# Optimization experiments

Hardware: AMD Instinct MI355X
Metric: run time of the kernel (lower is better)

The kernel has to match this reference:

```python
import jax, jax.numpy as jnp
import numpy as np

B, S, H = 32, 2048, 1024


def setup_inputs() -> dict:
    key = jax.random.key(0)
    k1, k2, k3, k4, k5 = jax.random.split(key, 5)
    # scale linear weights like torch default init (~U(-1/sqrt(fan_in),..)); normal*small is fine for a numeric baseline
    return {
        "hidden": jax.random.normal(k1, (B, H), dtype=jnp.float32),
        "encoder_outputs": jax.random.normal(k2, (B, S, H), dtype=jnp.float32),
        "attn_w": jax.random.normal(k3, (H, 2 * H), dtype=jnp.float32) * (1.0 / np.sqrt(2 * H)),
        "attn_b": jax.random.normal(k4, (H,), dtype=jnp.float32) * (1.0 / np.sqrt(2 * H)),
        "v_w": jax.random.normal(k5, (1, H), dtype=jnp.float32) * (1.0 / np.sqrt(H)),
    }


def reference(hidden, encoder_outputs, attn_w, attn_b, v_w):
    # hidden: [B,H]; encoder_outputs: [B,S,H]
    # torch: cat((hidden repeated over S, enc), dim=2) @ attn_w.T + attn_b
    # Split attn_w columns: first H cols act on hidden, last H cols on enc.
    # Avoids materializing the repeated/concatenated [B,S,2H] tensor.
    Hdim = hidden.shape[-1]
    Wh = attn_w[:, :Hdim]   # [H, H] applied to hidden
    We = attn_w[:, Hdim:]   # [H, H] applied to encoder outputs
    # [B,1,H] + [B,S,H] + [H] -> tanh -> [B,S,H]
    e = jnp.tanh((hidden @ Wh.T)[:, None, :] + jnp.einsum('bsh,kh->bsk', encoder_outputs, We) + attn_b)
    scores = jnp.einsum('bsh,h->bs', e, v_w[0])          # [B,S], v has no bias
    attn_weights = jax.nn.softmax(scores, axis=1)        # softmax over source positions (dim=1)
    context = jnp.einsum('bs,bsh->bh', attn_weights, encoder_outputs)  # [B,H]
    output = jnp.concatenate([context, hidden], axis=1)  # [B,2H]
    return output, attn_weights[..., None]               # match torch shapes: [B,2H], [B,S,1]
```

## Files before the change

### kernel.cpp

```cpp
#include <hip/hip_runtime.h>
#include <stdint.h>

#define BATCH 32
#define SEQ   2048
#define HDIM  1024

typedef short short8 __attribute__((ext_vector_type(8)));
typedef float f32x4 __attribute__((ext_vector_type(4)));

__device__ __forceinline__ unsigned short f2b(float f) {
    unsigned u = __float_as_uint(f);
    u += 0x7FFFu + ((u >> 16) & 1u);
    return (unsigned short)(u >> 16);
}
__device__ __forceinline__ unsigned pk_bf16(float a, float b) {
    return __builtin_amdgcn_perm(__float_as_uint(b), __float_as_uint(a), 0x07060302u);
}
__device__ __forceinline__ float fast_tanh(float x) {
    float ex = __expf(2.0f * x);
    return 1.0f - 2.0f / (ex + 1.0f);
}
__device__ __forceinline__ void gl2lds16(const unsigned short* g, unsigned short* l) {
    __builtin_amdgcn_global_load_lds(
        (const __attribute__((address_space(1))) unsigned int*)g,
        (__attribute__((address_space(3))) unsigned int*)l, 16, 0, 0);
}

__global__ __launch_bounds__(256) void prep_kernel(
    const float* __restrict__ hidden, const float* __restrict__ attn_w,
    const float* __restrict__ attn_b, unsigned short* __restrict__ we_bf,
    float* __restrict__ qb, float* __restrict__ scores) {
    int k = blockIdx.x;
    int tid = threadIdx.x;

    if (tid < 64) scores[(size_t)k * 64 + tid] = 0.0f;

    {
        const float4* src = (const float4*)(attn_w + (size_t)k * 2048 + 1024);
        float4 v = src[tid];
        ushort4 o;
        o.x = f2b(v.x); o.y = f2b(v.y); o.z = f2b(v.z); o.w = f2b(v.w);
        ((ushort4*)(we_bf + (size_t)k * HDIM))[tid] = o;
    }

    float part[BATCH];
#pragma unroll
    for (int b = 0; b < BATCH; ++b) part[b] = 0.0f;
    const float* wrow = attn_w + (size_t)k * 2048;
    for (int h = tid; h < HDIM; h += 256) {
        float w = wrow[h];
#pragma unroll
        for (int b = 0; b < BATCH; ++b) part[b] += w * hidden[b * HDIM + h];
    }
    __shared__ float red[4][BATCH];
    int lane = tid & 63, wv = tid >> 6;
#pragma unroll
    for (int b = 0; b < BATCH; ++b) {
        float v = part[b];
        v += __shfl_xor(v, 1);  v += __shfl_xor(v, 2);  v += __shfl_xor(v, 4);
        v += __shfl_xor(v, 8);  v += __shfl_xor(v, 16); v += __shfl_xor(v, 32);
        if (lane == 0) red[wv][b] = v;
    }
    __syncthreads();
    if (tid < BATCH) {
        float v = red[0][tid] + red[1][tid] + red[2][tid] + red[3][tid] + attn_b[k];
        qb[(size_t)tid * HDIM + k] = v;
    }
}

__global__ __launch_bounds__(256) void convert_kernel(
    const float* __restrict__ enc, unsigned short* __restrict__ enc_bf) {
    int id = blockIdx.x;
    int m = id >> 2, g = id & 3;
    int tid = threadIdx.x;
    int r = tid >> 1, h = tid & 1;
    const float* src = enc + ((size_t)m * 128 + r) * HDIM;
    int r7 = r & 7;
#pragma unroll
    for (int k4 = 0; k4 < 4; ++k4) {
        int kt = g * 4 + k4;
        unsigned short* img =
            enc_bf + ((size_t)m * 16 + kt) * 8192 + r * 64 + h * 32;
#pragma unroll
        for (int p = 0; p < 4; ++p) {
            int c = (4 * h + p) ^ r7;
            const float4* s = (const float4*)(src + kt * 64 + c * 8);
            float4 x = s[0], y = s[1];
            uint4 o;
            o.x = pk_bf16(x.x, x.y); o.y = pk_bf16(x.z, x.w);
            o.z = pk_bf16(y.x, y.y); o.w = pk_bf16(y.z, y.w);
            *(uint4*)(img + p * 8) = o;
        }
    }
}

__global__ __launch_bounds__(256, 3) void score_gemm_kernel(
    const unsigned short* __restrict__ enc_bf,
    const unsigned short* __restrict__ we_bf,
    const float* __restrict__ qb, const float* __restrict__ v_w,
    float* __restrict__ scores) {
    __shared__ __align__(16) unsigned short As[8192];
    __shared__ __align__(16) unsigned short Bs[8192];

    int tid  = threadIdx.x;
    int lane = tid & 63, w = tid >> 6;
    int wm = w & 1, wn = w >> 1;
    int i15 = lane & 15, q = lane >> 4;

    int raw   = blockIdx.x;
    int i     = raw >> 3;
    int ntile = i & 7;
    int mtile = (raw & 7) * 64 + (i >> 3);
    int n0 = ntile * 128;
    long gm0 = (long)mtile * 128;
    int b = mtile >> 4;

    int brow_in = lane >> 3;
    int bchunk  = (lane & 7) ^ ((lane >> 3) & 7);
    const unsigned short* Bg =
        we_bf + (size_t)(n0 + w * 32 + brow_in) * HDIM + bchunk * 8;
    unsigned short* Bd = Bs + (w * 32) * 64 + lane * 8;

    const unsigned short* Atile = enc_bf + (size_t)mtile * 16 * 8192;
    int aoff = w * 2048 + lane * 8;

    f32x4 acc[4][4];
#pragma unroll
    for (int mt = 0; mt < 4; ++mt)
#pragma unroll
        for (int nt = 0; nt < 4; ++nt) acc[mt][nt] = (f32x4)0.0f;

    int arow0 = wm * 64 + i15;
    int brow0 = wn * 64 + i15;

#define STAGE(KT) do {                                                        \
        const unsigned short* bsrc = Bg + (size_t)(KT) * 64;                  \
        gl2lds16(bsrc,                     Bd);                               \
        gl2lds16(bsrc + (size_t)8  * HDIM, Bd + 512);                         \
        gl2lds16(bsrc + (size_t)16 * HDIM, Bd + 1024);                        \
        gl2lds16(bsrc + (size_t)24 * HDIM, Bd + 1536);                        \
        const unsigned short* asrc = Atile + (size_t)(KT) * 8192 + aoff;      \
        unsigned short* adst = As + aoff;                                     \
        gl2lds16(asrc,        adst);                                          \
        gl2lds16(asrc + 512,  adst + 512);                                    \
        gl2lds16(asrc + 1024, adst + 1024);                                   \
        gl2lds16(asrc + 1536, adst + 1536);                                   \
    } while (0)

    STAGE(0);
    __syncthreads();

    for (int kt = 0; kt < 16; ++kt) {
#pragma unroll
        for (int kk = 0; kk < 2; ++kk) {
            int xr = ((kk * 4 + q) ^ (i15 & 7)) * 8;
            short8 af[4], bf[4];
#pragma unroll
            for (int mt = 0; mt < 4; ++mt)
                af[mt] = *(const short8*)(As + (arow0 + mt * 16) * 64 + xr);
#pragma unroll
            for (int nt = 0; nt < 4; ++nt)
                bf[nt] = *(const short8*)(Bs + (brow0 + nt * 16) * 64 + xr);
#pragma unroll
            for (int mt = 0; mt < 4; ++mt)
#pragma unroll
                for (int nt = 0; nt < 4; ++nt)
                    acc[mt][nt] = __builtin_amdgcn_mfma_f32_16x16x32_bf16(
                        af[mt], bf[nt], acc[mt][nt], 0, 0, 0);
        }
        if (kt < 15) {
            __syncthreads();
            STAGE(kt + 1);
            __syncthreads();
        }
    }
#undef STAGE

    float sc[4][4];
#pragma unroll
    for (int mt = 0; mt < 4; ++mt)
#pragma unroll
        for (int r = 0; r < 4; ++r) sc[mt][r] = 0.0f;

#pragma unroll
    for (int nt = 0; nt < 4; ++nt) {
        int n = n0 + wn * 64 + nt * 16 + i15;
        float qv = qb[(size_t)b * HDIM + n];
        float vv = v_w[n];
#pragma unroll
        for (int mt = 0; mt < 4; ++mt)
#pragma unroll
            for (int r = 0; r < 4; ++r)
                sc[mt][r] += vv * fast_tanh(acc[mt][nt][r] + qv);
    }
#pragma unroll
    for (int mt = 0; mt < 4; ++mt)
#pragma unroll
        for (int r = 0; r < 4; ++r) {
            float v = sc[mt][r];
            v += __shfl_xor(v, 1); v += __shfl_xor(v, 2);
            v += __shfl_xor(v, 4); v += __shfl_xor(v, 8);
            if (i15 == 0)
                atomicAdd(&scores[gm0 + wm * 64 + mt * 16 + q * 4 + r], v);
        }
}

__global__ __launch_bounds__(256) void softmax_kernel(
    const float* __restrict__ scores, const float* __restrict__ hidden,
    float* out) {
    int b = blockIdx.x, tid = threadIdx.x;
    const float* srow = scores + (size_t)b * SEQ;
    __shared__ float redm[4];
    __shared__ float reds[4];
    int lane = tid & 63, wv = tid >> 6;

    float loc[8];
    float m = -1e30f;
#pragma unroll
    for (int i = 0; i < 8; ++i) {
        loc[i] = srow[tid + i * 256];
        m = fmaxf(m, loc[i]);
    }
#pragma unroll
    for (int d = 1; d < 64; d <<= 1) m = fmaxf(m, __shfl_xor(m, d));
    if (lane == 0) redm[wv] = m;
    __syncthreads();
    m = fmaxf(fmaxf(redm[0], redm[1]), fmaxf(redm[2], redm[3]));

    float sum = 0.0f;
#pragma unroll
    for (int i = 0; i < 8; ++i) {
        float e = __expf(loc[i] - m);
        loc[i] = e;
        sum += e;
    }
#pragma unroll
    for (int d = 1; d < 64; d <<= 1) sum += __shfl_xor(sum, d);
    if (lane == 0) reds[wv] = sum;
    __syncthreads();
    sum = reds[0] + reds[1] + reds[2] + reds[3];
    float inv = 1.0f / sum;

#pragma unroll
    for (int i = 0; i < 8; ++i)
        out[BATCH * SEQ + (size_t)b * SEQ + tid + i * 256] = loc[i] * inv;

    for (int i = tid; i < HDIM; i += 256) {
        out[(size_t)b * 2048 + i] = 0.0f;
        out[(size_t)b * 2048 + 1024 + i] = hidden[(size_t)b * HDIM + i];
    }
}

__global__ __launch_bounds__(256) void context_kernel(
    const float* __restrict__ enc, const float* __restrict__ weights_src,
    float* out) {
    int id = blockIdx.x;
    int scid = id & 15, b = id >> 4;
    int tid = threadIdx.x;
    __shared__ float wl[128];
    if (tid < 128)
        wl[tid] = weights_src[BATCH * SEQ + (size_t)b * SEQ + scid * 128 + tid];
    __syncthreads();
    const float* ebase = enc + ((size_t)(b * SEQ + scid * 128)) * HDIM + tid * 4;
    float a0 = 0.f, a1 = 0.f, a2 = 0.f, a3 = 0.f;
    float b0 = 0.f, b1 = 0.f, b2 = 0.f, b3 = 0.f;
#pragma unroll 4
    for (int s = 0; s < 64; ++s) {
        float4 e0 = *(const float4*)(ebase + (size_t)s * HDIM);
        float4 e1 = *(const float4*)(ebase + (size_t)(s + 64) * HDIM);
        float w0 = wl[s], w1 = wl[s + 64];
        a0 += w0 * e0.x; a1 += w0 * e0.y; a2 += w0 * e0.z; a3 += w0 * e0.w;
        b0 += w1 * e1.x; b1 += w1 * e1.y; b2 += w1 * e1.z; b3 += w1 * e1.w;
    }
    float* o = out + (size_t)b * 2048 + tid * 4;
    atomicAdd(o + 0, a0 + b0); atomicAdd(o + 1, a1 + b1);
    atomicAdd(o + 2, a2 + b2); atomicAdd(o + 3, a3 + b3);
}

extern "C" void kernel_launch(void* const* d_in, const int* in_sizes, int n_in,
                              void* d_out, int out_size, void* d_ws, size_t ws_size,
                              hipStream_t stream) {
    const float* hidden = (const float*)d_in[0];
    const float* enc    = (const float*)d_in[1];
    const float* attn_w = (const float*)d_in[2];
    const float* attn_b = (const float*)d_in[3];
    const float* v_w    = (const float*)d_in[4];
    float* out = (float*)d_out;

    char* ws = (char*)d_ws;
    unsigned short* enc_bf = (unsigned short*)ws;
    unsigned short* we_bf  = (unsigned short*)(ws + (size_t)134217728);
    float* qb     = (float*)(ws + (size_t)134217728 + 2097152);
    float* scores = (float*)(ws + (size_t)134217728 + 2097152 + 131072);

    prep_kernel<<<1024, 256, 0, stream>>>(hidden, attn_w, attn_b, we_bf, qb, scores);
    convert_kernel<<<2048, 256, 0, stream>>>(enc, enc_bf);
    score_gemm_kernel<<<4096, 256, 0, stream>>>(enc_bf, we_bf, qb, v_w, scores);
    softmax_kernel<<<32, 256, 0, stream>>>(scores, hidden, out);
    context_kernel<<<512, 256, 0, stream>>>(enc, out, out);
}
```

Baseline: 649.6 us.

## Merge prep and convert kernels, move softmax normalization into context kernel

Fuses the bf16 conversion of encoder outputs and the weight/query prep into one launch so the two independent workloads share a grid. The softmax kernel now only computes per-row max and inverse sum, and the context kernel recomputes the normalized weights and writes them out, dropping a full-row write and read. The GEMM launch bound goes from 3 to 5 blocks per CU, which may force register spilling.

```diff
diff --git a/kernel.cpp b/kernel.cpp
--- a/kernel.cpp
+++ b/kernel.cpp
@@ -26,13 +26,40 @@
         (__attribute__((address_space(3))) unsigned int*)l, 16, 0, 0);
 }
 
-__global__ __launch_bounds__(256) void prep_kernel(
+__global__ __launch_bounds__(256) void prep_convert_kernel(
     const float* __restrict__ hidden, const float* __restrict__ attn_w,
-    const float* __restrict__ attn_b, unsigned short* __restrict__ we_bf,
+    const float* __restrict__ attn_b, const float* __restrict__ enc,
+    unsigned short* __restrict__ we_bf, unsigned short* __restrict__ enc_bf,
     float* __restrict__ qb, float* __restrict__ scores) {
-    int k = blockIdx.x;
+    int bid = blockIdx.x;
     int tid = threadIdx.x;
-
+    __shared__ float red[4][BATCH];
+
+    if (bid < 2048) {
+        int m = bid >> 2, g = bid & 3;
+        int r = tid >> 1, h = tid & 1;
+        const float* src = enc + ((size_t)m * 128 + r) * HDIM;
+        int r7 = r & 7;
+#pragma unroll
+        for (int k4 = 0; k4 < 4; ++k4) {
+            int kt = g * 4 + k4;
+            unsigned short* img =
+                enc_bf + ((size_t)m * 16 + kt) * 8192 + r * 64 + h * 32;
+#pragma unroll
+            for (int p = 0; p < 4; ++p) {
+                int c = (4 * h + p) ^ r7;
+                const float4* s = (const float4*)(src + kt * 64 + c * 8);
+                float4 x = s[0], y = s[1];
+                uint4 o;
+                o.x = pk_bf16(x.x, x.y); o.y = pk_bf16(x.z, x.w);
+                o.z = pk_bf16(y.x, y.y); o.w = pk_bf16(y.z, y.w);
+                *(uint4*)(img + p * 8) = o;
+            }
+        }
+        return;
+    }
+
+    int k = bid - 2048;
     if (tid < 64) scores[(size_t)k * 64 + tid] = 0.0f;
 
     {
@@ -52,7 +79,6 @@
 #pragma unroll
         for (int b = 0; b < BATCH; ++b) part[b] += w * hidden[b * HDIM + h];
     }
-    __shared__ float red[4][BATCH];
     int lane = tid & 63, wv = tid >> 6;
 #pragma unroll
     for (int b = 0; b < BATCH; ++b) {
@@ -68,33 +94,7 @@
     }
 }
 
-__global__ __launch_bounds__(256) void convert_kernel(
-    const float* __restrict__ enc, unsigned short* __restrict__ enc_bf) {
-    int id = blockIdx.x;
-    int m = id >> 2, g = id & 3;
-    int tid = threadIdx.x;
-    int r = tid >> 1, h = tid & 1;
-    const float* src = enc + ((size_t)m * 128 + r) * HDIM;
-    int r7 = r & 7;
-#pragma unroll
-    for (int k4 = 0; k4 < 4; ++k4) {
-        int kt = g * 4 + k4;
-        unsigned short* img =
-            enc_bf + ((size_t)m * 16 + kt) * 8192 + r * 64 + h * 32;
-#pragma unroll
-        for (int p = 0; p < 4; ++p) {
-            int c = (4 * h + p) ^ r7;
-            const float4* s = (const float4*)(src + kt * 64 + c * 8);
-            float4 x = s[0], y = s[1];
-            uint4 o;
-            o.x = pk_bf16(x.x, x.y); o.y = pk_bf16(x.z, x.w);
-            o.z = pk_bf16(y.x, y.y); o.w = pk_bf16(y.z, y.w);
-            *(uint4*)(img + p * 8) = o;
-        }
-    }
-}
-
-__global__ __launch_bounds__(256, 3) void score_gemm_kernel(
+__global__ __launch_bounds__(256, 5) void score_gemm_kernel(
     const unsigned short* __restrict__ enc_bf,
     const unsigned short* __restrict__ we_bf,
     const float* __restrict__ qb, const float* __restrict__ v_w,
@@ -205,9 +205,9 @@
         }
 }
 
-__global__ __launch_bounds__(256) void softmax_kernel(
+__global__ __launch_bounds__(256) void softmax_stats_kernel(
     const float* __restrict__ scores, const float* __restrict__ hidden,
-    float* out) {
+    float* __restrict__ stats, float* out) {
     int b = blockIdx.x, tid = threadIdx.x;
     const float* srow = scores + (size_t)b * SEQ;
     __shared__ float redm[4];
@@ -229,21 +229,16 @@
 
     float sum = 0.0f;
 #pragma unroll
-    for (int i = 0; i < 8; ++i) {
-        float e = __expf(loc[i] - m);
-        loc[i] = e;
-        sum += e;
-    }
+    for (int i = 0; i < 8; ++i) sum += __expf(loc[i] - m);
 #pragma unroll
     for (int d = 1; d < 64; d <<= 1) sum += __shfl_xor(sum, d);
     if (lane == 0) reds[wv] = sum;
     __syncthreads();
-    sum = reds[0] + reds[1] + reds[2] + reds[3];
-    float inv = 1.0f / sum;
-
-#pragma unroll
-    for (int i = 0; i < 8; ++i)
-        out[BATCH * SEQ + (size_t)b * SEQ + tid + i * 256] = loc[i] * inv;
+    if (tid == 0) {
+        float s = reds[0] + reds[1] + reds[2] + reds[3];
+        stats[2 * b]     = m;
+        stats[2 * b + 1] = 1.0f / s;
+    }
 
     for (int i = tid; i < HDIM; i += 256) {
         out[(size_t)b * 2048 + i] = 0.0f;
@@ -252,14 +247,19 @@
 }
 
 __global__ __launch_bounds__(256) void context_kernel(
-    const float* __restrict__ enc, const float* __restrict__ weights_src,
-    float* out) {
+    const float* __restrict__ enc, const float* __restrict__ scores,
+    const float* __restrict__ stats, float* out) {
     int id = blockIdx.x;
     int scid = id & 15, b = id >> 4;
     int tid = threadIdx.x;
     __shared__ float wl[128];
-    if (tid < 128)
-        wl[tid] = weights_src[BATCH * SEQ + (size_t)b * SEQ + scid * 128 + tid];
+    float m = stats[2 * b], inv = stats[2 * b + 1];
+    if (tid < 128) {
+        float s = scores[(size_t)b * SEQ + scid * 128 + tid];
+        float wgt = __expf(s - m) * inv;
+        wl[tid] = wgt;
+        out[BATCH * SEQ + (size_t)b * SEQ + scid * 128 + tid] = wgt;
+    }
     __syncthreads();
     const float* ebase = enc + ((size_t)(b * SEQ + scid * 128)) * HDIM + tid * 4;
     float a0 = 0.f, a1 = 0.f, a2 = 0.f, a3 = 0.f;
@@ -292,10 +292,11 @@
     unsigned short* we_bf  = (unsigned short*)(ws + (size_t)134217728);
     float* qb     = (float*)(ws + (size_t)134217728 + 2097152);
     float* scores = (float*)(ws + (size_t)134217728 + 2097152 + 131072);
-
-    prep_kernel<<<1024, 256, 0, stream>>>(hidden, attn_w, attn_b, we_bf, qb, scores);
-    convert_kernel<<<2048, 256, 0, stream>>>(enc, enc_bf);
+    float* stats  = (float*)(ws + (size_t)134217728 + 2097152 + 131072 + 262144);
+
+    prep_convert_kernel<<<3072, 256, 0, stream>>>(hidden, attn_w, attn_b, enc,
+                                                  we_bf, enc_bf, qb, scores);
     score_gemm_kernel<<<4096, 256, 0, stream>>>(enc_bf, we_bf, qb, v_w, scores);
-    softmax_kernel<<<32, 256, 0, stream>>>(scores, hidden, out);
-    context_kernel<<<512, 256, 0, stream>>>(enc, out, out);
-}
+    softmax_stats_kernel<<<32, 256, 0, stream>>>(scores, hidden, stats, out);
+    context_kernel<<<512, 256, 0, stream>>>(enc, scores, stats, out);
+}
```

Result: faster. 630.6 us (-2.9%).
